# Performance work log

Measured on AMD Instinct MI355X. Metric: run time of the kernel, lower is better.

The kernel has to match this reference:

```python
import jax, jax.numpy as jnp
import numpy as np

N = 50000          # nodes
E = 800000         # edges
H = 160            # hidden_dim = 32*5
HC = 32            # hidden_dim // 5 per-feature encoder width
LM = 768           # lm_input_dim
NUM_REL = 2
LEAK = 0.01        # nn.LeakyReLU default negative_slope


def leaky_relu(v):
    return jnp.where(v >= 0, v, LEAK * v)


def setup_inputs() -> dict:
    key = jax.random.key(0)
    ks = jax.random.split(key, 32)

    def lin(k, din, dout):
        kw, _ = jax.random.split(k)
        s = 1.0 / np.sqrt(din)
        W = jax.random.uniform(kw, (din, dout), jnp.float32, -s, s)
        b = jnp.zeros((dout,), jnp.float32)
        return W, b

    inp = {}
    inp["pre_x"] = jax.random.normal(ks[0], (N, LM), jnp.float32)
    inp["x"] = jnp.zeros((N, H), jnp.float32)  # dead input (overwritten in forward)
    inp["edge_index"] = jax.random.randint(ks[1], (2, E), 0, N, jnp.int32)
    inp["edge_type"] = jax.random.randint(ks[2], (E,), 0, NUM_REL, jnp.int32)
    inp["num_prop"] = jax.random.normal(ks[3], (N, 6), jnp.float32)
    inp["num_category"] = jax.random.normal(ks[4], (N, 11), jnp.float32)
    inp["des_tensor"] = jax.random.normal(ks[5], (N, LM), jnp.float32)
    inp["tweet_tensor"] = jax.random.normal(ks[6], (N, LM), jnp.float32)

    inp["W_np"], inp["b_np"] = lin(ks[7], 6, HC)
    inp["W_nc"], inp["b_nc"] = lin(ks[8], 11, HC)
    inp["W_des"], inp["b_des"] = lin(ks[9], LM, HC)
    inp["W_text"], inp["b_text"] = lin(ks[10], LM, HC)
    inp["W_tweet"], inp["b_tweet"] = lin(ks[11], LM, HC)
    inp["W_in"], inp["b_in"] = lin(ks[12], H, H)

    s = 1.0 / np.sqrt(H)
    inp["W_rel1"] = jax.random.uniform(ks[13], (NUM_REL, H, H), jnp.float32, -s, s)
    inp["W_root1"], inp["b_conv1"] = lin(ks[14], H, H)
    inp["W_rel2"] = jax.random.uniform(ks[15], (NUM_REL, H, H), jnp.float32, -s, s)
    inp["W_root2"], inp["b_conv2"] = lin(ks[16], H, H)

    inp["W_o1"], inp["b_o1"] = lin(ks[17], H, 80)
    inp["W_o2"], inp["b_o2"] = lin(ks[18], 80, 2)
    return inp


def rgcn_conv(h, src, dst, edge_type, W_rel, W_root, b):
    # PyG RGCNConv: per-relation mean aggregation + root transform + bias.
    out = h @ W_root + b
    for r in range(NUM_REL):
        w = (edge_type == r).astype(h.dtype)              # [E]
        msg = (h @ W_rel[r])[src] * w[:, None]            # [E, H] gather of transformed feats
        summed = jax.ops.segment_sum(msg, dst, num_segments=N)
        cnt = jax.ops.segment_sum(w, dst, num_segments=N)
        out = out + summed / jnp.maximum(cnt, 1.0)[:, None]
    return out


def reference(pre_x, x, edge_index, edge_type, num_prop, num_category, des_tensor,
              tweet_tensor, W_np, b_np, W_nc, b_nc, W_des, b_des, W_text, b_text,
              W_tweet, b_tweet, W_in, b_in, W_rel1, W_root1, b_conv1,
              W_rel2, W_root2, b_conv2, W_o1, b_o1, W_o2, b_o2):
    # Dropout is identity at inference.
    n = leaky_relu(num_prop @ W_np + b_np)
    c = leaky_relu(num_category @ W_nc + b_nc)
    d = leaky_relu(des_tensor @ W_des + b_des)
    tw = leaky_relu(tweet_tensor @ W_text + b_text)
    pre_t = leaky_relu(pre_x @ W_tweet + b_tweet)
    h = jnp.concatenate((n, c, d, tw, pre_t), axis=1)     # [N, 160]
    h = leaky_relu(h @ W_in + b_in)

    src, dst = edge_index[0], edge_index[1]
    h = rgcn_conv(h, src, dst, edge_type, W_rel1, W_root1, b_conv1)
    h = rgcn_conv(h, src, dst, edge_type, W_rel2, W_root2, b_conv2)

    em = leaky_relu(h @ W_o1 + b_o1)                      # [N, 80]
    out = em @ W_o2 + b_o2                                # [N, 2]
    return out, em
```

## Files before the change

kernel.cpp:

```cpp
#include <hip/hip_runtime.h>

#define NN 50000
#define EE 800000
#define HH 160
#define LMD 768
#define NBLK 196

typedef __attribute__((ext_vector_type(8))) short s8;
typedef __attribute__((ext_vector_type(4))) float f4;

__device__ __forceinline__ float lrelu(float v){ return v >= 0.f ? v : 0.01f*v; }

__device__ __forceinline__ short f2b(float f){
  unsigned int u = __float_as_uint(f);
  unsigned int r = (u + 0x7fffu + ((u >> 16) & 1u)) >> 16;
  return (short)r;
}
__device__ __forceinline__ float b2f(short s){
  return __uint_as_float(((unsigned int)(unsigned short)s) << 16);
}

struct WD { const float* s; short* d; int K; int C; int ldd; };
struct WDs { WD w[11]; };
__global__ __launch_bounds__(256) void wt_k(WDs ds)
{
  WD w = ds.w[blockIdx.y];
  int idx = blockIdx.x*256 + threadIdx.x;
  if (idx < w.K * w.C) {
    int k = idx / w.C, c = idx - k*w.C;
    w.d[(size_t)c*w.ldd + k] = f2b(w.s[idx]);
  }
}

__global__ __launch_bounds__(256) void enc_small_k(
    const float* __restrict__ npx, const float* __restrict__ ncx,
    const float* __restrict__ Wnp, const float* __restrict__ bnp,
    const float* __restrict__ Wnc, const float* __restrict__ bnc,
    short* __restrict__ out)
{
  int gid = blockIdx.x*256 + threadIdx.x;
  int row = gid >> 6, c = gid & 63;
  if (row >= NN) return;
  float acc;
  if (c < 32) {
    acc = bnp[c];
    #pragma unroll
    for (int k = 0; k < 6; ++k) acc += npx[row*6+k]*Wnp[k*32+c];
  } else {
    int cc = c - 32;
    acc = bnc[cc];
    #pragma unroll
    for (int k = 0; k < 11; ++k) acc += ncx[row*11+k]*Wnc[k*32+cc];
  }
  out[(size_t)row*HH + c] = f2b(lrelu(acc));
}

template<int C, bool XBF>
__global__ __launch_bounds__(256) void mgemm_k(
    const void* __restrict__ Xv, int ldx,
    const short* __restrict__ WT, const float* __restrict__ bias,
    short* __restrict__ outb, int ldo, int K, int leaky)
{
  constexpr int NT = C/16;
  __shared__ __attribute__((aligned(16))) short Xs[128*40];
  __shared__ __attribute__((aligned(16))) short Ws[C*40];
  const int t = threadIdx.x;
  const int r0 = blockIdx.x*128;
  const int w = t >> 6, L = t & 63;
  const int lm = L & 15, lq = L >> 4;

  f4 acc[2][NT];
  #pragma unroll
  for (int i = 0; i < 2; ++i)
    #pragma unroll
    for (int j = 0; j < NT; ++j) acc[i][j] = (f4){0.f,0.f,0.f,0.f};

  for (int k0 = 0; k0 < K; k0 += 32) {
    for (int i = t; i < 512; i += 256) {
      int row = i >> 2, kg = i & 3;
      int gr = r0 + row;
      s8 v;
      if (gr < NN) {
        if (XBF) {
          v = *(const s8*)((const short*)Xv + (size_t)gr*ldx + k0 + kg*8);
        } else {
          const float* xp = (const float*)Xv + (size_t)gr*ldx + k0 + kg*8;
          float4 a = *(const float4*)xp;
          float4 b = *(const float4*)(xp+4);
          v[0]=f2b(a.x); v[1]=f2b(a.y); v[2]=f2b(a.z); v[3]=f2b(a.w);
          v[4]=f2b(b.x); v[5]=f2b(b.y); v[6]=f2b(b.z); v[7]=f2b(b.w);
        }
      } else {
        v = (s8){0,0,0,0,0,0,0,0};
      }
      *(s8*)&Xs[row*40 + kg*8] = v;
    }
    for (int i = t; i < C*4; i += 256) {
      int c = i >> 2, kg = i & 3;
      *(s8*)&Ws[c*40 + kg*8] = *(const s8*)(WT + (size_t)c*K + k0 + kg*8);
    }
    __syncthreads();
    s8 a0 = *(const s8*)&Xs[(w*32 + lm)*40 + lq*8];
    s8 a1 = *(const s8*)&Xs[(w*32 + 16 + lm)*40 + lq*8];
    #pragma unroll
    for (int j = 0; j < NT; ++j) {
      s8 bf = *(const s8*)&Ws[(j*16 + lm)*40 + lq*8];
      acc[0][j] = __builtin_amdgcn_mfma_f32_16x16x32_bf16(a0, bf, acc[0][j], 0, 0, 0);
      acc[1][j] = __builtin_amdgcn_mfma_f32_16x16x32_bf16(a1, bf, acc[1][j], 0, 0, 0);
    }
    __syncthreads();
  }

  #pragma unroll
  for (int i = 0; i < 2; ++i) {
    #pragma unroll
    for (int j = 0; j < NT; ++j) {
      int col = j*16 + lm;
      float bv = bias ? bias[col] : 0.f;
      #pragma unroll
      for (int r = 0; r < 4; ++r) {
        int gr = r0 + w*32 + i*16 + lq*4 + r;
        if (gr < NN) {
          float v = acc[i][j][r] + bv;
          if (leaky) v = lrelu(v);
          outb[(size_t)gr*ldo + col] = f2b(v);
        }
      }
    }
  }
}

__global__ __launch_bounds__(256) void head_k(
    const short* __restrict__ X,
    const short* __restrict__ WT, const float* __restrict__ bias,
    const float* __restrict__ W2, const float* __restrict__ b2,
    float* __restrict__ em, float* __restrict__ out)
{
  constexpr int C = 80, NT = 5;
  __shared__ __attribute__((aligned(16))) short Xs[128*40];
  __shared__ __attribute__((aligned(16))) short Ws[C*40];
  __shared__ float emS[128][81];
  const int t = threadIdx.x;
  const int r0 = blockIdx.x*128;
  const int w = t >> 6, L = t & 63;
  const int lm = L & 15, lq = L >> 4;

  f4 acc[2][NT];
  #pragma unroll
  for (int i = 0; i < 2; ++i)
    #pragma unroll
    for (int j = 0; j < NT; ++j) acc[i][j] = (f4){0.f,0.f,0.f,0.f};

  for (int k0 = 0; k0 < HH; k0 += 32) {
    for (int i = t; i < 512; i += 256) {
      int row = i >> 2, kg = i & 3;
      int gr = r0 + row;
      s8 v = (s8){0,0,0,0,0,0,0,0};
      if (gr < NN) v = *(const s8*)(X + (size_t)gr*HH + k0 + kg*8);
      *(s8*)&Xs[row*40 + kg*8] = v;
    }
    for (int i = t; i < C*4; i += 256) {
      int c = i >> 2, kg = i & 3;
      *(s8*)&Ws[c*40 + kg*8] = *(const s8*)(WT + (size_t)c*HH + k0 + kg*8);
    }
    __syncthreads();
    s8 a0 = *(const s8*)&Xs[(w*32 + lm)*40 + lq*8];
    s8 a1 = *(const s8*)&Xs[(w*32 + 16 + lm)*40 + lq*8];
    #pragma unroll
    for (int j = 0; j < NT; ++j) {
      s8 bf = *(const s8*)&Ws[(j*16 + lm)*40 + lq*8];
      acc[0][j] = __builtin_amdgcn_mfma_f32_16x16x32_bf16(a0, bf, acc[0][j], 0, 0, 0);
      acc[1][j] = __builtin_amdgcn_mfma_f32_16x16x32_bf16(a1, bf, acc[1][j], 0, 0, 0);
    }
    __syncthreads();
  }

  #pragma unroll
  for (int i = 0; i < 2; ++i) {
    #pragma unroll
    for (int j = 0; j < NT; ++j) {
      int col = j*16 + lm;
      float bv = bias[col];
      #pragma unroll
      for (int r = 0; r < 4; ++r) {
        int lr = w*32 + i*16 + lq*4 + r;
        int gr = r0 + lr;
        if (gr < NN) {
          float v = lrelu(acc[i][j][r] + bv);
          em[(size_t)gr*80 + col] = v;
          emS[lr][col] = v;
        }
      }
    }
  }
  __syncthreads();
  if (t < 128) {
    int gr = r0 + t;
    if (gr < NN) {
      float a0 = b2[0], a1 = b2[1];
      #pragma unroll
      for (int k = 0; k < 80; ++k) {
        float v = emS[t][k];
        a0 += v*W2[k*2]; a1 += v*W2[k*2+1];
      }
      out[gr*2] = a0; out[gr*2+1] = a1;
    }
  }
}

__global__ __launch_bounds__(256) void hist_k(
    const int* __restrict__ dst, const int* __restrict__ et, int* __restrict__ cnt2)
{
  int e = blockIdx.x*256 + threadIdx.x;
  if (e < EE) atomicAdd(&cnt2[et[e]*NN + dst[e]], 1);
}

__global__ __launch_bounds__(256) void inv_k(
    const int* __restrict__ cnt2, float* __restrict__ inv2, int* __restrict__ cntall)
{
  int i = blockIdx.x*256 + threadIdx.x;
  if (i >= NN) return;
  int c0 = cnt2[i], c1 = cnt2[NN + i];
  inv2[i]      = 1.f / (float)max(c0, 1);
  inv2[NN + i] = 1.f / (float)max(c1, 1);
  cntall[i] = c0 + c1;
}

__global__ __launch_bounds__(256) void scan1_k(
    const int* __restrict__ cntall, int* __restrict__ off1, int* __restrict__ partials)
{
  __shared__ int sh[256];
  int t = threadIdx.x;
  int i = blockIdx.x*256 + t;
  sh[t] = (i < NN) ? cntall[i] : 0;
  __syncthreads();
  for (int s = 1; s < 256; s <<= 1) {
    int add = (t >= s) ? sh[t-s] : 0;
    __syncthreads();
    sh[t] += add;
    __syncthreads();
  }
  if (i < NN) off1[i] = sh[t];
  if (t == 255) partials[blockIdx.x] = sh[255];
}

__global__ __launch_bounds__(256) void scan2_k(int* __restrict__ partials)
{
  __shared__ int sh[256];
  int t = threadIdx.x;
  sh[t] = (t < NBLK) ? partials[t] : 0;
  __syncthreads();
  for (int s = 1; s < 256; s <<= 1) {
    int add = (t >= s) ? sh[t-s] : 0;
    __syncthreads();
    sh[t] += add;
    __syncthreads();
  }
  if (t < NBLK) partials[t] = (t == 0) ? 0 : sh[t-1];
}

__global__ __launch_bounds__(256) void scan3_k(
    int* __restrict__ off, int* __restrict__ cursor, const int* __restrict__ partials)
{
  int i = blockIdx.x*256 + threadIdx.x;
  if (i < NN) {
    int v = off[i+1] + partials[i >> 8];
    off[i+1] = v;
    if (i + 1 < NN) cursor[i+1] = v;
  }
  if (i == 0) { off[0] = 0; cursor[0] = 0; }
}

__global__ __launch_bounds__(256) void scatter_k(
    const int* __restrict__ src, const int* __restrict__ dst, const int* __restrict__ et,
    int* __restrict__ cursor, int* __restrict__ elist)
{
  int e = blockIdx.x*256 + threadIdx.x;
  if (e >= EE) return;
  int d = dst[e];
  int pos = atomicAdd(&cursor[d], 1);
  elist[pos] = (src[e] << 1) | et[e];
}

__global__ __launch_bounds__(256) void aggregate_k(
    const int* __restrict__ off, const int* __restrict__ elist,
    const float* __restrict__ inv2, short* __restrict__ X)
{
  int gid = blockIdx.x*256 + threadIdx.x;
  int d = gid / 20, q = gid - d*20;
  if (d >= NN) return;
  int beg = off[d], end = off[d+1];
  float a0[8], a1[8];
  #pragma unroll
  for (int i = 0; i < 8; ++i) { a0[i] = 0.f; a1[i] = 0.f; }
  for (int p = beg; p < end; ++p) {
    int pk = elist[p];
    int s = pk >> 1;
    float m1 = (float)(pk & 1), m0 = 1.f - m1;
    s8 v = *(const s8*)(X + (size_t)s*480 + q*8);
    #pragma unroll
    for (int i = 0; i < 8; ++i) {
      float f = b2f(v[i]);
      a0[i] += f*m0; a1[i] += f*m1;
    }
  }
  float i0 = inv2[d], i1 = inv2[NN + d];
  s8 o0, o1;
  #pragma unroll
  for (int i = 0; i < 8; ++i) { o0[i] = f2b(a0[i]*i0); o1[i] = f2b(a1[i]*i1); }
  *(s8*)(X + (size_t)d*480 + 160 + q*8) = o0;
  *(s8*)(X + (size_t)d*480 + 320 + q*8) = o1;
}

extern "C" void kernel_launch(void* const* d_in, const int* in_sizes, int n_in,
                              void* d_out, int out_size, void* d_ws, size_t ws_size,
                              hipStream_t stream)
{
  const float* pre_x   = (const float*)d_in[0];
  const int*   eidx    = (const int*)d_in[2];
  const int*   etype   = (const int*)d_in[3];
  const float* num_prop= (const float*)d_in[4];
  const float* num_cat = (const float*)d_in[5];
  const float* des     = (const float*)d_in[6];
  const float* tweet   = (const float*)d_in[7];
  const float* W_np=(const float*)d_in[8],  *b_np=(const float*)d_in[9];
  const float* W_nc=(const float*)d_in[10], *b_nc=(const float*)d_in[11];
  const float* W_des=(const float*)d_in[12],*b_des=(const float*)d_in[13];
  const float* W_text=(const float*)d_in[14],*b_text=(const float*)d_in[15];
  const float* W_tweet=(const float*)d_in[16],*b_tweet=(const float*)d_in[17];
  const float* W_in=(const float*)d_in[18], *b_in=(const float*)d_in[19];
  const float* W_rel1=(const float*)d_in[20], *W_root1=(const float*)d_in[21], *b_c1=(const float*)d_in[22];
  const float* W_rel2=(const float*)d_in[23], *W_root2=(const float*)d_in[24], *b_c2=(const float*)d_in[25];
  const float* W_o1=(const float*)d_in[26], *b_o1=(const float*)d_in[27];
  const float* W_o2=(const float*)d_in[28], *b_o2=(const float*)d_in[29];

  float* out = (float*)d_out;
  float* em  = out + (size_t)NN*2;

  short* Acat = (short*)d_ws;
  short* X1   = Acat + (size_t)NN*HH;
  short* X2   = X1   + (size_t)NN*480;
  short* WT   = X2   + (size_t)NN*480;
  short* WT_des   = WT;
  short* WT_text  = WT +  24576;
  short* WT_tweet = WT +  49152;
  short* WT_in    = WT +  73728;
  short* WT_cat1  = WT +  99328;
  short* WT_cat2  = WT + 176128;
  short* WT_o1    = WT + 252928;

  int*   cnt2    = (int*)(WT + 265728);
  float* inv2    = (float*)(cnt2 + 2*NN);
  int*   cntall  = (int*)(inv2 + 2*NN);
  int*   off     = cntall + NN;
  int*   partials= off + NN + 1;
  int*   cursor  = partials + 256;
  int*   elist   = cursor + NN;

  const int* src = eidx;
  const int* dst = eidx + EE;

  WDs ds;
  ds.w[0]  = (WD){W_des,          WT_des,         LMD, 32, LMD};
  ds.w[1]  = (WD){W_text,         WT_text,        LMD, 32, LMD};
  ds.w[2]  = (WD){W_tweet,        WT_tweet,       LMD, 32, LMD};
  ds.w[3]  = (WD){W_in,           WT_in,          HH, HH, HH};
  ds.w[4]  = (WD){W_root1,        WT_cat1,        HH, HH, 480};
  ds.w[5]  = (WD){W_rel1,         WT_cat1 + 160,  HH, HH, 480};
  ds.w[6]  = (WD){W_rel1 + HH*HH, WT_cat1 + 320,  HH, HH, 480};
  ds.w[7]  = (WD){W_root2,        WT_cat2,        HH, HH, 480};
  ds.w[8]  = (WD){W_rel2,         WT_cat2 + 160,  HH, HH, 480};
  ds.w[9]  = (WD){W_rel2 + HH*HH, WT_cat2 + 320,  HH, HH, 480};
  ds.w[10] = (WD){W_o1,           WT_o1,          HH, 80, HH};
  wt_k<<<dim3(100, 11), 256, 0, stream>>>(ds);

  hipMemsetAsync(cnt2, 0, 2*NN*sizeof(int), stream);
  hist_k  <<<(EE+255)/256, 256, 0, stream>>>(dst, etype, cnt2);
  inv_k   <<<NBLK, 256, 0, stream>>>(cnt2, inv2, cntall);
  scan1_k <<<NBLK, 256, 0, stream>>>(cntall, off+1, partials);
  scan2_k <<<1,    256, 0, stream>>>(partials);
  scan3_k <<<NBLK, 256, 0, stream>>>(off, cursor, partials);
  scatter_k<<<(EE+255)/256, 256, 0, stream>>>(src, dst, etype, cursor, elist);

  enc_small_k<<<(NN*64+255)/256, 256, 0, stream>>>(num_prop, num_cat, W_np,b_np, W_nc,b_nc, Acat);
  const int GB = (NN + 127) / 128;
  mgemm_k<32,false><<<GB,256,0,stream>>>(des,   LMD, WT_des,   b_des,   Acat+64,  HH, LMD, 1);
  mgemm_k<32,false><<<GB,256,0,stream>>>(tweet, LMD, WT_text,  b_text,  Acat+96,  HH, LMD, 1);
  mgemm_k<32,false><<<GB,256,0,stream>>>(pre_x, LMD, WT_tweet, b_tweet, Acat+128, HH, LMD, 1);

  mgemm_k<160,true><<<GB,256,0,stream>>>(Acat, HH, WT_in, b_in, X1, 480, HH, 1);

  aggregate_k<<<(NN*20+255)/256, 256, 0, stream>>>(off, elist, inv2, X1);
  mgemm_k<160,true><<<GB,256,0,stream>>>(X1, 480, WT_cat1, b_c1, X2, 480, 480, 0);

  aggregate_k<<<(NN*20+255)/256, 256, 0, stream>>>(off, elist, inv2, X2);
  mgemm_k<160,true><<<GB,256,0,stream>>>(X2, 480, WT_cat2, b_c2, Acat, HH, 480, 0);

  head_k<<<GB,256,0,stream>>>(Acat, WT_o1, b_o1, W_o2, b_o2, em, out);
}
```

Before: 908.9 us.

## Prefetch GEMM tiles into registers, shrink row tiles, and fuse small launches

The GEMM kernel now uses 64-row tiles instead of 128, doubling the block count for better occupancy across CUs. It also prefetches the next K-slice of X and W into registers while the current slice is consumed from shared memory. The three encoder GEMMs are merged into one launch over a 2D grid, the counter memset is folded into the weight-transpose kernel, and inv_k is fused into scan1. The aggregation loop is unrolled by two so each thread has more gathers in flight. Smaller tiles mean each weight tile is reloaded by twice as many blocks, and the extra prefetch registers may reduce occupancy.

New measurement: 819.2 us. -9.9%, faster.

```diff
diff --git a/kernel.cpp b/kernel.cpp
--- a/kernel.cpp
+++ b/kernel.cpp
@@ -5,6 +5,7 @@
 #define HH 160
 #define LMD 768
 #define NBLK 196
+#define GB64 782
 
 typedef __attribute__((ext_vector_type(8))) short s8;
 typedef __attribute__((ext_vector_type(4))) float f4;
@@ -21,9 +22,18 @@
 }
 
 struct WD { const float* s; short* d; int K; int C; int ldd; };
-struct WDs { WD w[11]; };
+struct WDs { WD w[11]; int* cnt2; };
 __global__ __launch_bounds__(256) void wt_k(WDs ds)
 {
+  if (blockIdx.y == 11) {
+    int idx = blockIdx.x*256 + threadIdx.x;
+    #pragma unroll
+    for (int j = 0; j < 4; ++j) {
+      int i = idx + j*25600;
+      if (i < 2*NN) ds.cnt2[i] = 0;
+    }
+    return;
+  }
   WD w = ds.w[blockIdx.y];
   int idx = blockIdx.x*256 + threadIdx.x;
   if (idx < w.K * w.C) {
@@ -56,78 +66,108 @@
 }
 
 template<int C, bool XBF>
-__global__ __launch_bounds__(256) void mgemm_k(
+__device__ __forceinline__ void gemm_body(
     const void* __restrict__ Xv, int ldx,
     const short* __restrict__ WT, const float* __restrict__ bias,
-    short* __restrict__ outb, int ldo, int K, int leaky)
+    short* __restrict__ outb, int ldo, int K, int leaky, int r0)
 {
   constexpr int NT = C/16;
-  __shared__ __attribute__((aligned(16))) short Xs[128*40];
+  constexpr int NW = (C*4 + 255)/256;
+  __shared__ __attribute__((aligned(16))) short Xs[64*40];
   __shared__ __attribute__((aligned(16))) short Ws[C*40];
   const int t = threadIdx.x;
-  const int r0 = blockIdx.x*128;
   const int w = t >> 6, L = t & 63;
   const int lm = L & 15, lq = L >> 4;
-
-  f4 acc[2][NT];
-  #pragma unroll
-  for (int i = 0; i < 2; ++i)
-    #pragma unroll
-    for (int j = 0; j < NT; ++j) acc[i][j] = (f4){0.f,0.f,0.f,0.f};
+  const int srow = t >> 2, skg = t & 3;
+  const int gr = r0 + srow;
+
+  f4 acc[NT];
+  #pragma unroll
+  for (int j = 0; j < NT; ++j) acc[j] = (f4){0.f,0.f,0.f,0.f};
+
+  s8 xv = (s8){0,0,0,0,0,0,0,0};
+  s8 wv[NW];
+
+  if (gr < NN) {
+    if (XBF) {
+      xv = *(const s8*)((const short*)Xv + (size_t)gr*ldx + skg*8);
+    } else {
+      const float* xp = (const float*)Xv + (size_t)gr*ldx + skg*8;
+      float4 a = *(const float4*)xp, b = *(const float4*)(xp+4);
+      xv[0]=f2b(a.x); xv[1]=f2b(a.y); xv[2]=f2b(a.z); xv[3]=f2b(a.w);
+      xv[4]=f2b(b.x); xv[5]=f2b(b.y); xv[6]=f2b(b.z); xv[7]=f2b(b.w);
+    }
+  }
+  #pragma unroll
+  for (int s = 0; s < NW; ++s) {
+    int i = t + s*256;
+    if (i < C*4) { int c = i>>2, kg = i&3; wv[s] = *(const s8*)(WT + (size_t)c*K + kg*8); }
+  }
 
   for (int k0 = 0; k0 < K; k0 += 32) {
-    for (int i = t; i < 512; i += 256) {
-      int row = i >> 2, kg = i & 3;
-      int gr = r0 + row;
-      s8 v;
+    if (k0) __syncthreads();
+    *(s8*)&Xs[srow*40 + skg*8] = xv;
+    #pragma unroll
+    for (int s = 0; s < NW; ++s) {
+      int i = t + s*256;
+      if (i < C*4) { int c = i>>2, kg = i&3; *(s8*)&Ws[c*40 + kg*8] = wv[s]; }
+    }
+    __syncthreads();
+    int kn = k0 + 32;
+    if (kn < K) {
       if (gr < NN) {
         if (XBF) {
-          v = *(const s8*)((const short*)Xv + (size_t)gr*ldx + k0 + kg*8);
+          xv = *(const s8*)((const short*)Xv + (size_t)gr*ldx + kn + skg*8);
         } else {
-          const float* xp = (const float*)Xv + (size_t)gr*ldx + k0 + kg*8;
-          float4 a = *(const float4*)xp;
-          float4 b = *(const float4*)(xp+4);
-          v[0]=f2b(a.x); v[1]=f2b(a.y); v[2]=f2b(a.z); v[3]=f2b(a.w);
-          v[4]=f2b(b.x); v[5]=f2b(b.y); v[6]=f2b(b.z); v[7]=f2b(b.w);
+          const float* xp = (const float*)Xv + (size_t)gr*ldx + kn + skg*8;
+          float4 a = *(const float4*)xp, b = *(const float4*)(xp+4);
+          xv[0]=f2b(a.x); xv[1]=f2b(a.y); xv[2]=f2b(a.z); xv[3]=f2b(a.w);
+          xv[4]=f2b(b.x); xv[5]=f2b(b.y); xv[6]=f2b(b.z); xv[7]=f2b(b.w);
         }
-      } else {
-        v = (s8){0,0,0,0,0,0,0,0};
       }
-      *(s8*)&Xs[row*40 + kg*8] = v;
-    }
-    for (int i = t; i < C*4; i += 256) {
-      int c = i >> 2, kg = i & 3;
-      *(s8*)&Ws[c*40 + kg*8] = *(const s8*)(WT + (size_t)c*K + k0 + kg*8);
-    }
-    __syncthreads();
-    s8 a0 = *(const s8*)&Xs[(w*32 + lm)*40 + lq*8];
-    s8 a1 = *(const s8*)&Xs[(w*32 + 16 + lm)*40 + lq*8];
+      #pragma unroll
+      for (int s = 0; s < NW; ++s) {
+        int i = t + s*256;
+        if (i < C*4) { int c = i>>2, kg = i&3; wv[s] = *(const s8*)(WT + (size_t)c*K + kn + kg*8); }
+      }
+    }
+    s8 a = *(const s8*)&Xs[(w*16 + lm)*40 + lq*8];
     #pragma unroll
     for (int j = 0; j < NT; ++j) {
       s8 bf = *(const s8*)&Ws[(j*16 + lm)*40 + lq*8];
-      acc[0][j] = __builtin_amdgcn_mfma_f32_16x16x32_bf16(a0, bf, acc[0][j], 0, 0, 0);
-      acc[1][j] = __builtin_amdgcn_mfma_f32_16x16x32_bf16(a1, bf, acc[1][j], 0, 0, 0);
-    }
-    __syncthreads();
-  }
-
-  #pragma unroll
-  for (int i = 0; i < 2; ++i) {
-    #pragma unroll
-    for (int j = 0; j < NT; ++j) {
-      int col = j*16 + lm;
-      float bv = bias ? bias[col] : 0.f;
-      #pragma unroll
-      for (int r = 0; r < 4; ++r) {
-        int gr = r0 + w*32 + i*16 + lq*4 + r;
-        if (gr < NN) {
-          float v = acc[i][j][r] + bv;
-          if (leaky) v = lrelu(v);
-          outb[(size_t)gr*ldo + col] = f2b(v);
-        }
+      acc[j] = __builtin_amdgcn_mfma_f32_16x16x32_bf16(a, bf, acc[j], 0, 0, 0);
+    }
+  }
+
+  #pragma unroll
+  for (int j = 0; j < NT; ++j) {
+    int col = j*16 + lm;
+    float bv = bias ? bias[col] : 0.f;
+    #pragma unroll
+    for (int r = 0; r < 4; ++r) {
+      int go = r0 + w*16 + lq*4 + r;
+      if (go < NN) {
+        float v = acc[j][r] + bv;
+        if (leaky) v = lrelu(v);
+        outb[(size_t)go*ldo + col] = f2b(v);
       }
     }
   }
+}
+
+struct Enc3 { const float* X[3]; const short* WT[3]; const float* B[3]; short* out[3]; };
+__global__ __launch_bounds__(256) void enc3_k(Enc3 e)
+{
+  int j = blockIdx.y;
+  gemm_body<32,false>(e.X[j], LMD, e.WT[j], e.B[j], e.out[j], HH, LMD, 1, blockIdx.x*64);
+}
+
+__global__ __launch_bounds__(256) void dgemm_k(
+    const short* __restrict__ X, int ldx,
+    const short* __restrict__ WT, const float* __restrict__ bias,
+    short* __restrict__ outb, int ldo, int K, int leaky)
+{
+  gemm_body<160,true>(X, ldx, WT, bias, outb, ldo, K, leaky, blockIdx.x*64);
 }
 
 __global__ __launch_bounds__(256) void head_k(
@@ -215,24 +255,20 @@
   if (e < EE) atomicAdd(&cnt2[et[e]*NN + dst[e]], 1);
 }
 
-__global__ __launch_bounds__(256) void inv_k(
-    const int* __restrict__ cnt2, float* __restrict__ inv2, int* __restrict__ cntall)
-{
-  int i = blockIdx.x*256 + threadIdx.x;
-  if (i >= NN) return;
-  int c0 = cnt2[i], c1 = cnt2[NN + i];
-  inv2[i]      = 1.f / (float)max(c0, 1);
-  inv2[NN + i] = 1.f / (float)max(c1, 1);
-  cntall[i] = c0 + c1;
-}
-
 __global__ __launch_bounds__(256) void scan1_k(
-    const int* __restrict__ cntall, int* __restrict__ off1, int* __restrict__ partials)
+    const int* __restrict__ cnt2, float* __restrict__ inv2,
+    int* __restrict__ off1, int* __restrict__ partials)
 {
   __shared__ int sh[256];
   int t = threadIdx.x;
   int i = blockIdx.x*256 + t;
-  sh[t] = (i < NN) ? cntall[i] : 0;
+  int c0 = 0, c1 = 0;
+  if (i < NN) {
+    c0 = cnt2[i]; c1 = cnt2[NN + i];
+    inv2[i]      = 1.f / (float)max(c0, 1);
+    inv2[NN + i] = 1.f / (float)max(c1, 1);
+  }
+  sh[t] = c0 + c1;
   __syncthreads();
   for (int s = 1; s < 256; s <<= 1) {
     int add = (t >= s) ? sh[t-s] : 0;
@@ -293,11 +329,24 @@
   float a0[8], a1[8];
   #pragma unroll
   for (int i = 0; i < 8; ++i) { a0[i] = 0.f; a1[i] = 0.f; }
-  for (int p = beg; p < end; ++p) {
+  int p = beg;
+  for (; p + 2 <= end; p += 2) {
+    int pk0 = elist[p], pk1 = elist[p+1];
+    s8 v0 = *(const s8*)(X + (size_t)(pk0 >> 1)*480 + q*8);
+    s8 v1 = *(const s8*)(X + (size_t)(pk1 >> 1)*480 + q*8);
+    float m10 = (float)(pk0 & 1), m00 = 1.f - m10;
+    float m11 = (float)(pk1 & 1), m01 = 1.f - m11;
+    #pragma unroll
+    for (int i = 0; i < 8; ++i) {
+      float f0 = b2f(v0[i]), f1 = b2f(v1[i]);
+      a0[i] += f0*m00 + f1*m01;
+      a1[i] += f0*m10 + f1*m11;
+    }
+  }
+  if (p < end) {
     int pk = elist[p];
-    int s = pk >> 1;
+    s8 v = *(const s8*)(X + (size_t)(pk >> 1)*480 + q*8);
     float m1 = (float)(pk & 1), m0 = 1.f - m1;
-    s8 v = *(const s8*)(X + (size_t)s*480 + q*8);
     #pragma unroll
     for (int i = 0; i < 8; ++i) {
       float f = b2f(v[i]);
@@ -351,8 +400,7 @@
 
   int*   cnt2    = (int*)(WT + 265728);
   float* inv2    = (float*)(cnt2 + 2*NN);
-  int*   cntall  = (int*)(inv2 + 2*NN);
-  int*   off     = cntall + NN;
+  int*   off     = (int*)(inv2 + 2*NN);
   int*   partials= off + NN + 1;
   int*   cursor  = partials + 256;
   int*   elist   = cursor + NN;
@@ -372,29 +420,29 @@
   ds.w[8]  = (WD){W_rel2,         WT_cat2 + 160,  HH, HH, 480};
   ds.w[9]  = (WD){W_rel2 + HH*HH, WT_cat2 + 320,  HH, HH, 480};
   ds.w[10] = (WD){W_o1,           WT_o1,          HH, 80, HH};
-  wt_k<<<dim3(100, 11), 256, 0, stream>>>(ds);
-
-  hipMemsetAsync(cnt2, 0, 2*NN*sizeof(int), stream);
+  ds.cnt2  = cnt2;
+  wt_k<<<dim3(100, 12), 256, 0, stream>>>(ds);
+
   hist_k  <<<(EE+255)/256, 256, 0, stream>>>(dst, etype, cnt2);
-  inv_k   <<<NBLK, 256, 0, stream>>>(cnt2, inv2, cntall);
-  scan1_k <<<NBLK, 256, 0, stream>>>(cntall, off+1, partials);
+  scan1_k <<<NBLK, 256, 0, stream>>>(cnt2, inv2, off+1, partials);
   scan2_k <<<1,    256, 0, stream>>>(partials);
   scan3_k <<<NBLK, 256, 0, stream>>>(off, cursor, partials);
   scatter_k<<<(EE+255)/256, 256, 0, stream>>>(src, dst, etype, cursor, elist);
 
   enc_small_k<<<(NN*64+255)/256, 256, 0, stream>>>(num_prop, num_cat, W_np,b_np, W_nc,b_nc, Acat);
-  const int GB = (NN + 127) / 128;
-  mgemm_k<32,false><<<GB,256,0,stream>>>(des,   LMD, WT_des,   b_des,   Acat+64,  HH, LMD, 1);
-  mgemm_k<32,false><<<GB,256,0,stream>>>(tweet, LMD, WT_text,  b_text,  Acat+96,  HH, LMD, 1);
-  mgemm_k<32,false><<<GB,256,0,stream>>>(pre_x, LMD, WT_tweet, b_tweet, Acat+128, HH, LMD, 1);
-
-  mgemm_k<160,true><<<GB,256,0,stream>>>(Acat, HH, WT_in, b_in, X1, 480, HH, 1);
+  Enc3 e3;
+  e3.X[0]=des;     e3.WT[0]=WT_des;   e3.B[0]=b_des;   e3.out[0]=Acat+64;
+  e3.X[1]=tweet;   e3.WT[1]=WT_text;  e3.B[1]=b_text;  e3.out[1]=Acat+96;
+  e3.X[2]=pre_x;   e3.WT[2]=WT_tweet; e3.B[2]=b_tweet; e3.out[2]=Acat+128;
+  enc3_k<<<dim3(GB64, 3), 256, 0, stream>>>(e3);
+
+  dgemm_k<<<GB64,256,0,stream>>>(Acat, HH, WT_in, b_in, X1, 480, HH, 1);
 
   aggregate_k<<<(NN*20+255)/256, 256, 0, stream>>>(off, elist, inv2, X1);
-  mgemm_k<160,true><<<GB,256,0,stream>>>(X1, 480, WT_cat1, b_c1, X2, 480, 480, 0);
+  dgemm_k<<<GB64,256,0,stream>>>(X1, 480, WT_cat1, b_c1, X2, 480, 480, 0);
 
   aggregate_k<<<(NN*20+255)/256, 256, 0, stream>>>(off, elist, inv2, X2);
-  mgemm_k<160,true><<<GB,256,0,stream>>>(X2, 480, WT_cat2, b_c2, Acat, HH, 480, 0);
-
-  head_k<<<GB,256,0,stream>>>(Acat, WT_o1, b_o1, W_o2, b_o2, em, out);
-}
+  dgemm_k<<<GB64,256,0,stream>>>(X2, 480, WT_cat2, b_c2, Acat, HH, 480, 0);
+
+  head_k<<<(NN+127)/128,256,0,stream>>>(Acat, WT_o1, b_o1, W_o2, b_o2, em, out);
+}
```
